# Kernel optimization log

Measured on AMD Instinct MI355X. Metric: run time of the kernel, lower is better.

The kernel has to match this reference:

```python
import jax, jax.numpy as jnp
import numpy as np

B, S, D, E = 4, 1024, 1024, 4
HID = 2816  # multiple_of * ceil(int(2*4*D/3) / multiple_of), multiple_of=256
COND = 1024  # min(D, 1024)
NORM_EPS = 1e-5  # block norms
LN_EPS = 1e-5    # q_norm/k_norm default eps


def setup_inputs() -> dict:
    key = jax.random.key(0)
    ks = jax.random.split(key, 16)
    w = lambda i, shape: jax.random.normal(ks[i], shape, jnp.float32) * 0.02
    return {
        'x': jax.random.normal(ks[0], (B, S, D), jnp.float32),
        'freqs_cis': jax.random.normal(ks[1], (S, 32), jnp.float32),  # unused by the block
        'adaln_input': jax.random.normal(ks[2], (B, COND), jnp.float32),
        'wq': w(3, (D, D)), 'wk': w(4, (D, D)), 'wv': w(5, (D, D)), 'wo': w(6, (D, D)),
        'q_norm_w': jnp.ones((D,), jnp.float32), 'q_norm_b': jnp.zeros((D,), jnp.float32),
        'k_norm_w': jnp.ones((D,), jnp.float32), 'k_norm_b': jnp.zeros((D,), jnp.float32),
        'attn_norm_w': jnp.ones((D,), jnp.float32), 'attn_norm_b': jnp.zeros((D,), jnp.float32),
        'ffn_norm_w': jnp.ones((D,), jnp.float32), 'ffn_norm_b': jnp.zeros((D,), jnp.float32),
        'w1': w(7, (E, D, HID)), 'w2': w(8, (E, HID, D)), 'w3': w(9, (E, D, HID)),
        'router_w': w(10, (D, E)), 'router_b': jnp.zeros((E,), jnp.float32),
        'ada_w': w(11, (COND, 6 * D)), 'ada_b': jnp.zeros((6 * D,), jnp.float32),
    }


def _ln(x, w, b, eps):
    mu = jnp.mean(x, -1, keepdims=True)
    var = jnp.mean((x - mu) ** 2, -1, keepdims=True)
    return (x - mu) * jax.lax.rsqrt(var + eps) * w + b


def _attention(x, wq, wk, wv, wo, qn_w, qn_b, kn_w, kn_b):
    # NOTE: this module attends over the FEATURE dim (no head split, no 1/sqrt(d) scale):
    # xq,xk,xv are permuted to [B, D, S]; scores are [B, D, D].
    q = _ln(x @ wq, qn_w, qn_b, LN_EPS)
    k = _ln(x @ wk, kn_w, kn_b, LN_EPS)
    v = x @ wv
    scores = jnp.einsum('bsd,bse->bde', q, k)          # [B, D, D]
    attn = jax.nn.softmax(scores, axis=-1)
    out = jnp.einsum('bde,bse->bsd', attn, v)          # [B, S, D]
    return out @ wo


def _moe(x, w1, w2, w3, router_w, router_b):
    logits = x @ router_w + router_b                   # [B, S, E]
    # F.normalize default dim=1 -> L2-normalize along the SEQUENCE dim (faithful quirk)
    nrm = jnp.sqrt(jnp.sum(logits * logits, axis=1, keepdims=True))
    logits = logits / jnp.maximum(nrm, 1e-12)
    probs = jax.nn.softmax(logits, axis=-1)
    topw, topi = jax.lax.top_k(probs, 2)
    # dense combine weights [B,S,E]: identical math to the masked gather/scatter dispatch
    combine = jnp.sum(jax.nn.one_hot(topi, E, dtype=x.dtype) * topw[..., None], axis=-2)
    h1 = jnp.einsum('bsd,edh->ebsh', x, w1)
    h3 = jnp.einsum('bsd,edh->ebsh', x, w3)
    out_e = jnp.einsum('ebsh,ehd->ebsd', jnp.sin(h1) * h3, w2)
    moe = jnp.einsum('bse,ebsd->bsd', combine, out_e)
    avg = jnp.mean(probs, axis=0)                      # [S, E] (mean over batch dim only)
    aux = jnp.sum((1.0 / E - avg) ** 2)
    return moe, aux


def reference(x, freqs_cis, adaln_input, wq, wk, wv, wo, q_norm_w, q_norm_b, k_norm_w,
              k_norm_b, attn_norm_w, attn_norm_b, ffn_norm_w, ffn_norm_b, w1, w2, w3,
              router_w, router_b, ada_w, ada_b):
    ada = jax.nn.silu(adaln_input) @ ada_w + ada_b     # [B, 6D]
    shift_msa, scale_msa, gate_msa, shift_mlp, scale_mlp, gate_mlp = jnp.split(ada, 6, axis=1)
    h = _ln(x, attn_norm_w, attn_norm_b, NORM_EPS)
    h = h * (1.0 + scale_msa[:, None, :]) + shift_msa[:, None, :]
    x = x + gate_msa[:, None, :] * _attention(h, wq, wk, wv, wo, q_norm_w, q_norm_b, k_norm_w, k_norm_b)
    h = _ln(x, ffn_norm_w, ffn_norm_b, NORM_EPS)
    h = h * (1.0 + scale_mlp[:, None, :]) + shift_mlp[:, None, :]
    # MoE path REPLACES x (no residual, gate_mlp unused) — faithful to the source
    x, aux = _moe(h, w1, w2, w3, router_w, router_b)
    return x, aux
```

## Files before the change

kernel.cpp:

```cpp
#include <hip/hip_runtime.h>
#include <hip/hip_bf16.h>
#include <math.h>

#define BB 4
#define SS 1024
#define DD 1024
#define EE 4
#define HID 2816
#define HC 1408
#define SIXD 6144
#define NSLOT 8704
#define NMB 68

typedef __bf16 v8bf __attribute__((ext_vector_type(8)));
typedef float  v4f  __attribute__((ext_vector_type(4)));

__device__ __forceinline__ ushort f2bf(float f) {
    union { float f; unsigned u; } v; v.f = f;
    unsigned r = v.u + 0x7fff + ((v.u >> 16) & 1);
    return (ushort)(r >> 16);
}
__device__ __forceinline__ float bf2f(ushort u) {
    union { unsigned u; float f; } v; v.u = ((unsigned)u) << 16;
    return v.f;
}
__device__ __forceinline__ void split_bf(float x, ushort& h, ushort& l) {
    h = f2bf(x);
    l = f2bf(x - bf2f(h));
}
__device__ __forceinline__ void gload16(const void* g, void* l) {
    __builtin_amdgcn_global_load_lds((const __attribute__((address_space(1))) void*)g,
                                     (__attribute__((address_space(3))) void*)l, 16, 0, 0);
}
template<int N> __device__ __forceinline__ void wait_vm() {
    __builtin_amdgcn_s_waitcnt((N & 15) | (0x7 << 4) | (0xF << 8) | ((N >> 4) << 14));
}

__device__ __forceinline__ void xcd_remap(int& bx, int& by) {
    const int gx = gridDim.x, gy = gridDim.y;
    const int nwg = gx * gy;
    const int wid = bx + gx * by;
    const int q = nwg >> 3, r = nwg & 7;
    const int xcd = wid & 7, loc = wid >> 3;
    const int pos = (xcd < r) ? (xcd * (q + 1) + loc)
                              : (r * (q + 1) + (xcd - r) * q + loc);
    bx = pos % gx; by = pos / gx;
}

__device__ __forceinline__ void xcd_remap_cm(int& bx, int& by) {
    const int gx = gridDim.x, gy = gridDim.y;
    const int nwg = gx * gy;
    const int wid = bx + gx * by;
    const int q = nwg >> 3, r = nwg & 7;
    const int xcd = wid & 7, loc = wid >> 3;
    const int pos = (xcd < r) ? (xcd * (q + 1) + loc)
                              : (r * (q + 1) + (xcd - r) * q + loc);
    bx = pos / gy; by = pos % gy;
}

__device__ __forceinline__ void moe_remap(int& bx, int& by) {
    const int gx = gridDim.x, gy = gridDim.y;
    const int total = gx * gy;
    const int wid = bx + gx * by;
    if ((total & 7) || (gx & 1)) { xcd_remap(bx, by); return; }
    const int q = total >> 3;
    const int pos = (wid & 7) * q + (wid >> 3);
    const int NG = gx >> 1;
    const int gh = NG * gy;
    const int nh = pos / gh, r = pos % gh;
    by = r / NG;
    bx = nh * NG + (r % NG);
}

template<int EPI, bool SPLIT>
__global__ __launch_bounds__(256, 2) void mgemm(
    const ushort* __restrict__ Ah, const ushort* __restrict__ Al,
    const ushort* __restrict__ Bh, const ushort* __restrict__ Bl,
    void* __restrict__ Cv, ushort* __restrict__ C2,
    const float* __restrict__ f1, const float* __restrict__ f2,
    int K, int lda, int ldb, int ldc,
    long sA, long sB, long sC)
{
    constexpr int STG = SPLIT ? 12288 : 6144;
    constexpr int BH  = SPLIT ? 8192 : 4096;
    constexpr int L   = SPLIT ? 6 : 3;
    __shared__ __align__(16) ushort smem[3 * STG];

    const int tid  = threadIdx.x;
    const int wv   = tid >> 6, lane = tid & 63;

    int bx = blockIdx.x, by = blockIdx.y;
    xcd_remap(bx, by);
    const int n0 = bx * 64;
    const int m0 = by * 128;
    const long zA = (long)blockIdx.z * sA;
    const long zB = (long)blockIdx.z * sB;
    const long zC = (long)blockIdx.z * sC;

    const int lrow = tid >> 2;
    const int skq  = ((tid & 3) ^ ((tid >> 3) & 3)) * 8;
    const int lm   = lane & 15;
    const int qs   = (((lane >> 4) ^ ((lm >> 1) & 3)) * 8);

    v4f acc[2][4];
    const v4f vzero = {0.f, 0.f, 0.f, 0.f};
    #pragma unroll
    for (int i = 0; i < 2; ++i)
        #pragma unroll
        for (int j = 0; j < 4; ++j) acc[i][j] = vzero;

    auto issue = [&](int kt, int st) {
        const long kk = (long)kt * 32 + skq;
        ushort* base = smem + st * STG;
        #pragma unroll
        for (int c = 0; c < 2; ++c) {
            const int row  = c * 64 + lrow;
            const int loff = (c * 64 + wv * 16) * 32;
            gload16(Ah + zA + (long)(m0 + row) * lda + kk, base + loff);
            if (SPLIT)
                gload16(Al + zA + (long)(m0 + row) * lda + kk, base + 4096 + loff);
        }
        {
            const int loff = wv * 16 * 32;
            gload16(Bh + zB + (long)(n0 + lrow) * ldb + kk, base + BH + loff);
            if (SPLIT)
                gload16(Bl + zB + (long)(n0 + lrow) * ldb + kk, base + BH + 2048 + loff);
        }
    };

    const int nk = K / 32;
    issue(0, 0);
    if (nk > 1) issue(1, 1);
    for (int kt = 0; kt < nk; ++kt) {
        if (kt + 1 < nk) wait_vm<L>(); else wait_vm<0>();
        __builtin_amdgcn_s_barrier();
        if (kt + 2 < nk) issue(kt + 2, (kt + 2) % 3);
        const ushort* As = smem + (kt % 3) * STG;
        v8bf a[2], b[4];
        #pragma unroll
        for (int i = 0; i < 2; ++i) a[i] = *(const v8bf*)(As + (wv*32 + 16*i + lm) * 32 + qs);
        #pragma unroll
        for (int j = 0; j < 4; ++j) b[j] = *(const v8bf*)(As + BH + (16*j + lm) * 32 + qs);
        #pragma unroll
        for (int i = 0; i < 2; ++i)
            #pragma unroll
            for (int j = 0; j < 4; ++j)
                acc[i][j] = __builtin_amdgcn_mfma_f32_16x16x32_bf16(a[i], b[j], acc[i][j], 0, 0, 0);
        if (SPLIT) {
            v8bf al[2], bl[4];
            #pragma unroll
            for (int i = 0; i < 2; ++i) al[i] = *(const v8bf*)(As + 4096 + (wv*32 + 16*i + lm) * 32 + qs);
            #pragma unroll
            for (int j = 0; j < 4; ++j) bl[j] = *(const v8bf*)(As + BH + 2048 + (16*j + lm) * 32 + qs);
            #pragma unroll
            for (int i = 0; i < 2; ++i)
                #pragma unroll
                for (int j = 0; j < 4; ++j) {
                    acc[i][j] = __builtin_amdgcn_mfma_f32_16x16x32_bf16(a[i],  bl[j], acc[i][j], 0, 0, 0);
                    acc[i][j] = __builtin_amdgcn_mfma_f32_16x16x32_bf16(al[i], b[j],  acc[i][j], 0, 0, 0);
                }
        }
    }

    const int r0 = (lane >> 4) * 4;
    #pragma unroll
    for (int i = 0; i < 2; ++i) {
        #pragma unroll
        for (int j = 0; j < 4; ++j) {
            const int colg = n0 + 16*j + lm;
            #pragma unroll
            for (int r = 0; r < 4; ++r) {
                const long rowg = (long)(m0 + wv*32 + 16*i + r0 + r);
                const long idx  = zC + rowg * ldc + colg;
                const float val = acc[i][j][r];
                if (EPI == 0) {
                    ((float*)Cv)[idx] = val;
                } else if (EPI == 2) {
                    ((float*)Cv)[idx] = f1[idx] + f2[(rowg >> 10) * SIXD + 2048 + colg] * val;
                } else if (EPI == 5) {
                    ushort h, l; split_bf(val, h, l);
                    ((ushort*)Cv)[idx] = h;
                    C2[idx] = l;
                }
            }
        }
    }
}

__global__ __launch_bounds__(256, 2) void mgemm_qkv(
    const ushort* __restrict__ Ah, const ushort* __restrict__ Al,
    const ushort* __restrict__ Bqh, const ushort* __restrict__ Bql,
    const ushort* __restrict__ Bkh, const ushort* __restrict__ Bkl,
    const ushort* __restrict__ Bvh, const ushort* __restrict__ Bvl,
    float* __restrict__ Cq, float* __restrict__ Ck,
    ushort* __restrict__ Cvh, ushort* __restrict__ Cvl)
{
    constexpr int STG = 20480;
    __shared__ __align__(16) ushort smem[2 * STG];

    const int tid  = threadIdx.x;
    const int wv   = tid >> 6, lane = tid & 63;

    int bx = blockIdx.x, by = blockIdx.y;
    xcd_remap(bx, by);
    const int n0 = bx * 64, m0 = by * 128;

    const int lrow = tid >> 2;
    const int skq  = ((tid & 3) ^ ((tid >> 3) & 3)) * 8;
    const int lm   = lane & 15;
    const int qs   = (((lane >> 4) ^ ((lm >> 1) & 3)) * 8);

    const ushort* Bh_[3] = {Bqh, Bkh, Bvh};
    const ushort* Bl_[3] = {Bql, Bkl, Bvl};

    v4f aq[2][4], ak[2][4], av[2][4];
    const v4f vzero = {0.f, 0.f, 0.f, 0.f};
    #pragma unroll
    for (int i = 0; i < 2; ++i)
        #pragma unroll
        for (int j = 0; j < 4; ++j) { aq[i][j] = vzero; ak[i][j] = vzero; av[i][j] = vzero; }

    auto issue = [&](int kt, int st) {
        const long kk = (long)kt * 32 + skq;
        ushort* base = smem + st * STG;
        #pragma unroll
        for (int c = 0; c < 2; ++c) {
            const int row  = c * 64 + lrow;
            const int loff = (c * 64 + wv * 16) * 32;
            gload16(Ah + (long)(m0 + row) * 1024 + kk, base + loff);
            gload16(Al + (long)(m0 + row) * 1024 + kk, base + 4096 + loff);
        }
        const int loff = wv * 16 * 32;
        #pragma unroll
        for (int m = 0; m < 3; ++m) {
            gload16(Bh_[m] + (long)(n0 + lrow) * 1024 + kk, base + 8192 + m * 4096 + loff);
            gload16(Bl_[m] + (long)(n0 + lrow) * 1024 + kk, base + 8192 + m * 4096 + 2048 + loff);
        }
    };

    issue(0, 0);
    #pragma unroll 1
    for (int kt = 0; kt < 32; ++kt) {
        const int stg = kt & 1;
        if (kt) __builtin_amdgcn_s_barrier();
        const bool hasNext = (kt + 1 < 32);
        if (hasNext) issue(kt + 1, stg ^ 1);
        if (hasNext) wait_vm<10>(); else wait_vm<0>();
        __builtin_amdgcn_s_barrier();
        const ushort* As = smem + stg * STG;
        v8bf a[2], alo[2];
        #pragma unroll
        for (int i = 0; i < 2; ++i) {
            a[i]   = *(const v8bf*)(As + (wv*32 + 16*i + lm) * 32 + qs);
            alo[i] = *(const v8bf*)(As + 4096 + (wv*32 + 16*i + lm) * 32 + qs);
        }
        auto mat = [&](const ushort* Bs, v4f (&acc)[2][4]) {
            v8bf b[4], bl[4];
            #pragma unroll
            for (int j = 0; j < 4; ++j) {
                b[j]  = *(const v8bf*)(Bs + (16*j + lm) * 32 + qs);
                bl[j] = *(const v8bf*)(Bs + 2048 + (16*j + lm) * 32 + qs);
            }
            #pragma unroll
            for (int i = 0; i < 2; ++i)
                #pragma unroll
                for (int j = 0; j < 4; ++j) {
                    acc[i][j] = __builtin_amdgcn_mfma_f32_16x16x32_bf16(a[i],   b[j],  acc[i][j], 0, 0, 0);
                    acc[i][j] = __builtin_amdgcn_mfma_f32_16x16x32_bf16(a[i],   bl[j], acc[i][j], 0, 0, 0);
                    acc[i][j] = __builtin_amdgcn_mfma_f32_16x16x32_bf16(alo[i], b[j],  acc[i][j], 0, 0, 0);
                }
        };
        mat(As + 8192,        aq);
        mat(As + 8192 + 4096, ak);
        mat(As + 8192 + 8192, av);
    }

    const int r0 = (lane >> 4) * 4;
    #pragma unroll
    for (int i = 0; i < 2; ++i)
        #pragma unroll
        for (int j = 0; j < 4; ++j) {
            const int colg = n0 + 16*j + lm;
            #pragma unroll
            for (int r = 0; r < 4; ++r) {
                const long rowg = (long)(m0 + wv*32 + 16*i + r0 + r);
                const long idx  = rowg * 1024 + colg;
                Cq[idx] = aq[i][j][r];
                Ck[idx] = ak[i][j][r];
                ushort h, l; split_bf(av[i][j][r], h, l);
                Cvh[idx] = h;
                Cvl[idx] = l;
            }
        }
}

__global__ __launch_bounds__(512, 2) void mgemm_h1h3(
    const ushort* __restrict__ Ah, const ushort* __restrict__ B1,
    const ushort* __restrict__ B2, ushort* __restrict__ Cb,
    const int* __restrict__ tokidx, const int* __restrict__ mbe,
    const int* __restrict__ mbm, long sB)
{
    constexpr int STG = 12288;
    __shared__ __align__(16) ushort smem[3 * STG];

    const int tid  = threadIdx.x;
    const int wv   = tid >> 6, lane = tid & 63;
    const int wr   = wv >> 2, wc = wv & 3;

    int bx = blockIdx.x, by = blockIdx.y;
    xcd_remap_cm(bx, by);
    const int n0 = bx * 128;
    const int eexp = mbe[by];
    if (eexp < 0) return;
    const int m0 = mbm[by];
    const long zB = (long)eexp * sB;

    const int lrow = tid >> 2;
    const int skq  = ((tid & 3) ^ ((tid >> 3) & 3)) * 8;
    const int lm   = lane & 15;
    const int qs   = (((lane >> 4) ^ ((lm >> 1) & 3)) * 8);

    const int t = tokidx[m0 + lrow];
    const long arow = (t < 0) ? 0 : (long)t;

    v4f acc[4][2], acc2[4][2];
    const v4f vzero = {0.f, 0.f, 0.f, 0.f};
    #pragma unroll
    for (int i = 0; i < 4; ++i)
        #pragma unroll
        for (int j = 0; j < 2; ++j) { acc[i][j] = vzero; acc2[i][j] = vzero; }

    auto issue = [&](int kt, int st) {
        const long kk = (long)kt * 32 + skq;
        ushort* base = smem + st * STG;
        const int loff = wv * 16 * 32;
        gload16(Ah + arow * 1024 + kk, base + loff);
        gload16(B1 + zB + (long)(n0 + lrow) * 1024 + kk, base + 4096 + loff);
        gload16(B2 + zB + (long)(n0 + lrow) * 1024 + kk, base + 8192 + loff);
    };

    issue(0, 0);
    issue(1, 1);
    int s_cur = 0, s_nxt = 2;
    #pragma unroll 1
    for (int kt = 0; kt < 32; ++kt) {
        if (kt + 1 < 32) wait_vm<3>(); else wait_vm<0>();
        __builtin_amdgcn_s_barrier();
        if (kt + 2 < 32) issue(kt + 2, s_nxt);
        const ushort* As = smem + s_cur * STG;
        v8bf a[4], b1[2], b2[2];
        #pragma unroll
        for (int i = 0; i < 4; ++i) a[i] = *(const v8bf*)(As + (wr*64 + 16*i + lm) * 32 + qs);
        #pragma unroll
        for (int j = 0; j < 2; ++j) {
            b1[j] = *(const v8bf*)(As + 4096 + (wc*32 + 16*j + lm) * 32 + qs);
            b2[j] = *(const v8bf*)(As + 8192 + (wc*32 + 16*j + lm) * 32 + qs);
        }
        #pragma unroll
        for (int i = 0; i < 4; ++i)
            #pragma unroll
            for (int j = 0; j < 2; ++j) {
                acc[i][j]  = __builtin_amdgcn_mfma_f32_16x16x32_bf16(a[i], b1[j], acc[i][j],  0, 0, 0);
                acc2[i][j] = __builtin_amdgcn_mfma_f32_16x16x32_bf16(a[i], b2[j], acc2[i][j], 0, 0, 0);
            }
        s_cur = (s_cur == 2) ? 0 : s_cur + 1;
        s_nxt = (s_nxt == 2) ? 0 : s_nxt + 1;
    }

    const int r0 = (lane >> 4) * 4;
    #pragma unroll
    for (int i = 0; i < 4; ++i)
        #pragma unroll
        for (int j = 0; j < 2; ++j) {
            const int colg = n0 + wc*32 + 16*j + lm;
            #pragma unroll
            for (int r = 0; r < 4; ++r) {
                const long rowg = (long)(m0 + wr*64 + 16*i + r0 + r);
                Cb[rowg * HC + colg] = f2bf(sinf(acc[i][j][r]) * acc2[i][j][r]);
            }
        }
}

__global__ __launch_bounds__(256, 2) void mgemm_w2(
    const ushort* __restrict__ Ah, const ushort* __restrict__ Bh,
    float* __restrict__ Cv, const float* __restrict__ comb,
    const int* __restrict__ tokidx, const int* __restrict__ mbe,
    const int* __restrict__ mbm, long sB)
{
    constexpr int STG = 8192;
    __shared__ __align__(16) ushort smem[3 * STG];

    const int tid  = threadIdx.x;
    const int wv   = tid >> 6, lane = tid & 63;
    const int wr   = wv >> 1, wc = wv & 1;

    int bx = blockIdx.x, by = blockIdx.y;
    moe_remap(bx, by);
    const int n0 = bx * 128;
    const int eexp = mbe[by];
    if (eexp < 0) return;
    const int m0 = mbm[by];
    const long zB = (long)eexp * sB;

    const int lrow = tid >> 2;
    const int skq  = ((tid & 3) ^ ((tid >> 3) & 3)) * 8;
    const int lm   = lane & 15;
    const int qs   = (((lane >> 4) ^ ((lm >> 1) & 3)) * 8);

    v4f acc[4][4];
    const v4f vzero = {0.f, 0.f, 0.f, 0.f};
    #pragma unroll
    for (int i = 0; i < 4; ++i)
        #pragma unroll
        for (int j = 0; j < 4; ++j) acc[i][j] = vzero;

    auto issue = [&](int kt, int st) {
        const long kk = (long)kt * 32 + skq;
        ushort* base = smem + st * STG;
        #pragma unroll
        for (int c = 0; c < 2; ++c) {
            const int loff = (c * 64 + wv * 16) * 32;
            gload16(Ah + (long)(m0 + c * 64 + lrow) * HC + kk, base + loff);
            gload16(Bh + zB + (long)(n0 + c * 64 + lrow) * HC + kk, base + 4096 + loff);
        }
    };

    const int nk = HC / 32;
    issue(0, 0);
    issue(1, 1);
    int s_cur = 0, s_nxt = 2;
    #pragma unroll 1
    for (int kt = 0; kt < nk; ++kt) {
        if (kt + 1 < nk) wait_vm<4>(); else wait_vm<0>();
        __builtin_amdgcn_s_barrier();
        if (kt + 2 < nk) issue(kt + 2, s_nxt);
        const ushort* As = smem + s_cur * STG;
        v8bf a[4], b[4];
        #pragma unroll
        for (int i = 0; i < 4; ++i) a[i] = *(const v8bf*)(As + (wr*64 + 16*i + lm) * 32 + qs);
        #pragma unroll
        for (int j = 0; j < 4; ++j) b[j] = *(const v8bf*)(As + 4096 + (wc*64 + 16*j + lm) * 32 + qs);
        #pragma unroll
        for (int i = 0; i < 4; ++i)
            #pragma unroll
            for (int j = 0; j < 4; ++j)
                acc[i][j] = __builtin_amdgcn_mfma_f32_16x16x32_bf16(a[i], b[j], acc[i][j], 0, 0, 0);
        s_cur = (s_cur == 2) ? 0 : s_cur + 1;
        s_nxt = (s_nxt == 2) ? 0 : s_nxt + 1;
    }

    const int r0 = (lane >> 4) * 4;
    #pragma unroll
    for (int i = 0; i < 4; ++i)
        #pragma unroll
        for (int r = 0; r < 4; ++r) {
            const int rowg = m0 + wr*64 + 16*i + r0 + r;
            const int t = tokidx[rowg];
            if (t >= 0) {
                const float cw = comb[t * 4 + eexp];
                #pragma unroll
                for (int j = 0; j < 4; ++j)
                    atomicAdd(Cv + (long)t * 1024 + n0 + wc*64 + 16*j + lm, cw * acc[i][j][r]);
            }
        }
}

template<bool SP>
__global__ __launch_bounds__(256) void transp(
    const float* __restrict__ in, ushort* __restrict__ oh, ushort* __restrict__ ol,
    int ldin, int ldout, long sIn, long sOut)
{
    __shared__ float T[64][65];
    const int n0 = blockIdx.x * 64, k0 = blockIdx.y * 64;
    in += (long)blockIdx.z * sIn;
    oh += (long)blockIdx.z * sOut;
    if (SP) ol += (long)blockIdx.z * sOut;
    const int t = threadIdx.x;
    const int rr = t >> 4, c4 = (t & 15) * 4;
    #pragma unroll
    for (int p = 0; p < 4; ++p) {
        const int r = rr + p * 16;
        const float4 v = *(const float4*)(in + (long)(k0 + r) * ldin + n0 + c4);
        T[c4+0][r] = v.x; T[c4+1][r] = v.y; T[c4+2][r] = v.z; T[c4+3][r] = v.w;
    }
    __syncthreads();
    #pragma unroll
    for (int p = 0; p < 4; ++p) {
        const int idx = t + 256 * p;
        const int n = idx >> 4, c = (idx & 15) * 4;
        ushort4 wh, wl;
        float x0 = T[n][c], x1 = T[n][c+1], x2 = T[n][c+2], x3 = T[n][c+3];
        if (SP) {
            split_bf(x0, wh.x, wl.x); split_bf(x1, wh.y, wl.y);
            split_bf(x2, wh.z, wl.z); split_bf(x3, wh.w, wl.w);
        } else {
            wh.x = f2bf(x0); wh.y = f2bf(x1); wh.z = f2bf(x2); wh.w = f2bf(x3);
        }
        *(ushort4*)(oh + (long)(n0 + n) * ldout + k0 + c) = wh;
        if (SP) *(ushort4*)(ol + (long)(n0 + n) * ldout + k0 + c) = wl;
    }
}

__global__ __launch_bounds__(256) void ada_kernel(
    const float* __restrict__ adaln, const float* __restrict__ aw,
    const float* __restrict__ ab, float* __restrict__ ada)
{
    __shared__ float s[DD];
    const int b = blockIdx.y;
    const int tid = threadIdx.x;
    for (int i = tid; i < DD; i += 256) {
        const float v = adaln[(long)b * DD + i];
        s[i] = v / (1.f + expf(-v));
    }
    __syncthreads();
    const int n = blockIdx.x * 256 + tid;
    float acc = 0.f;
    for (int k = 0; k < DD; ++k) acc += s[k] * aw[(long)k * SIXD + n];
    ada[(long)b * SIXD + n] = acc + ab[n];
}

template<int OUT, bool MOD>
__global__ __launch_bounds__(256) void ln_kernel(
    const float* __restrict__ x, const float* __restrict__ w, const float* __restrict__ bias,
    const float* __restrict__ ada, int scale_off, int shift_off,
    float* __restrict__ o32, ushort* __restrict__ oh, ushort* __restrict__ ol, float eps)
{
    const int row = blockIdx.x;
    const int b = row >> 10;
    const int tid = threadIdx.x;
    const float* xr = x + (long)row * DD;
    float v[4]; float s = 0.f, q = 0.f;
    #pragma unroll
    for (int i = 0; i < 4; ++i) { v[i] = xr[tid + 256*i]; s += v[i]; q += v[i]*v[i]; }
    __shared__ float rs_[256], rq_[256];
    rs_[tid] = s; rq_[tid] = q; __syncthreads();
    for (int off = 128; off > 0; off >>= 1) {
        if (tid < off) { rs_[tid] += rs_[tid+off]; rq_[tid] += rq_[tid+off]; }
        __syncthreads();
    }
    const float mu  = rs_[0] * (1.f/DD);
    const float var = rq_[0] * (1.f/DD) - mu*mu;
    const float rstd = rsqrtf(var + eps);
    const float* ar = ada + (long)b * SIXD;
    #pragma unroll
    for (int i = 0; i < 4; ++i) {
        const int d = tid + 256*i;
        float y = (v[i] - mu) * rstd * w[d] + bias[d];
        if (MOD) y = y * (1.f + ar[scale_off + d]) + ar[shift_off + d];
        const long idx = (long)row * DD + d;
        if (OUT == 0) o32[idx] = y;
        else if (OUT == 1) { ushort h, l; split_bf(y, h, l); oh[idx] = h; ol[idx] = l; }
        else oh[idx] = f2bf(y);
    }
}

__global__ __launch_bounds__(256) void softmax_split(
    const float* __restrict__ in, ushort* __restrict__ oh, ushort* __restrict__ ol)
{
    const long row = blockIdx.x;
    const float* p = in + row * 1024;
    const int tid = threadIdx.x;
    float v[4]; float mx = -INFINITY;
    #pragma unroll
    for (int i = 0; i < 4; ++i) { v[i] = p[tid + 256*i]; mx = fmaxf(mx, v[i]); }
    __shared__ float red[256];
    red[tid] = mx; __syncthreads();
    for (int off = 128; off > 0; off >>= 1) {
        if (tid < off) red[tid] = fmaxf(red[tid], red[tid+off]);
        __syncthreads();
    }
    const float rowmax = red[0];
    __syncthreads();
    float s = 0.f;
    #pragma unroll
    for (int i = 0; i < 4; ++i) { v[i] = expf(v[i] - rowmax); s += v[i]; }
    red[tid] = s; __syncthreads();
    for (int off = 128; off > 0; off >>= 1) {
        if (tid < off) red[tid] += red[tid+off];
        __syncthreads();
    }
    const float inv = 1.f / red[0];
    #pragma unroll
    for (int i = 0; i < 4; ++i) {
        ushort h, l; split_bf(v[i] * inv, h, l);
        oh[row*1024 + tid + 256*i] = h;
        ol[row*1024 + tid + 256*i] = l;
    }
}

__global__ __launch_bounds__(256) void ln_router(
    const float* __restrict__ x2, const float* __restrict__ fw, const float* __restrict__ fb,
    const float* __restrict__ ada, const float* __restrict__ rw, const float* __restrict__ rb,
    float* __restrict__ logits, ushort* __restrict__ oh)
{
    const int row = blockIdx.x;
    const int b = row >> 10;
    const int tid = threadIdx.x;
    const float* xr = x2 + (long)row * DD;
    float v[4]; float s = 0.f, q = 0.f;
    #pragma unroll
    for (int i = 0; i < 4; ++i) { v[i] = xr[tid + 256*i]; s += v[i]; q += v[i]*v[i]; }
    __shared__ float rs_[256], rq_[256];
    rs_[tid] = s; rq_[tid] = q; __syncthreads();
    for (int off = 128; off > 0; off >>= 1) {
        if (tid < off) { rs_[tid] += rs_[tid+off]; rq_[tid] += rq_[tid+off]; }
        __syncthreads();
    }
    const float mu  = rs_[0] * (1.f/DD);
    const float var = rq_[0] * (1.f/DD) - mu*mu;
    const float rstd = rsqrtf(var + 1e-5f);
    const float* ar = ada + (long)b * SIXD;
    float acc[4] = {0.f, 0.f, 0.f, 0.f};
    #pragma unroll
    for (int i = 0; i < 4; ++i) {
        const int d = tid + 256*i;
        float h = (v[i] - mu) * rstd * fw[d] + fb[d];
        h = h * (1.f + ar[4096 + d]) + ar[3072 + d];
        oh[(long)row * DD + d] = f2bf(h);
        const float* r4 = rw + (long)d * 4;
        acc[0] += h*r4[0]; acc[1] += h*r4[1]; acc[2] += h*r4[2]; acc[3] += h*r4[3];
    }
    __syncthreads();
    __shared__ float red[256];
    for (int e = 0; e < EE; ++e) {
        red[tid] = acc[e]; __syncthreads();
        for (int off = 128; off > 0; off >>= 1) {
            if (tid < off) red[tid] += red[tid+off];
            __syncthreads();
        }
        if (tid == 0) logits[(long)row * EE + e] = red[0] + rb[e];
        __syncthreads();
    }
}

__global__ __launch_bounds__(1024) void router_all(
    const float* __restrict__ logits, float* __restrict__ comb,
    float* __restrict__ auxout, int* __restrict__ tokidx,
    int* __restrict__ mbe, int* __restrict__ mbm)
{
    __shared__ float pl[16384];
    __shared__ float red[1024];
    __shared__ float nrm_l[16];
    __shared__ int lc[4], loff[4], lpos[4];
    const int tid = threadIdx.x;
    const int wv = tid >> 6, ln = tid & 63;
    {
        const int b = wv >> 2, e = wv & 3;
        float s = 0.f;
        for (int it = 0; it < 16; ++it) {
            const float v = logits[(((long)b << 10) + ln + (it << 6)) * 4 + e];
            s += v * v;
        }
        for (int off = 32; off > 0; off >>= 1) s += __shfl_down(s, off, 64);
        if (ln == 0) nrm_l[wv] = fmaxf(sqrtf(s), 1e-12f);
    }
    if (tid < 4) lc[tid] = 0;
    __syncthreads();
    float cloc[4][4];
    const int rbase = tid * 4;
    for (int rr = 0; rr < 4; ++rr) {
        const int row = rbase + rr;
        const int b = row >> 10;
        float l[4], p[4];
        #pragma unroll
        for (int e = 0; e < 4; ++e) l[e] = logits[(long)row*4 + e] / nrm_l[b*4 + e];
        const float mx = fmaxf(fmaxf(l[0], l[1]), fmaxf(l[2], l[3]));
        float s = 0.f;
        #pragma unroll
        for (int e = 0; e < 4; ++e) { p[e] = expf(l[e] - mx); s += p[e]; }
        const float inv = 1.f / s;
        #pragma unroll
        for (int e = 0; e < 4; ++e) { p[e] *= inv; pl[row*4 + e] = p[e]; }
        int i1 = 0;
        #pragma unroll
        for (int e = 1; e < 4; ++e) if (p[e] > p[i1]) i1 = e;
        int i2 = (i1 == 0) ? 1 : 0;
        #pragma unroll
        for (int e = 0; e < 4; ++e) if (e != i1 && p[e] > p[i2]) i2 = e;
        #pragma unroll
        for (int e = 0; e < 4; ++e) {
            const float c = (e == i1) ? p[i1] : ((e == i2) ? p[i2] : 0.f);
            cloc[rr][e] = c;
            comb[(long)row*4 + e] = c;
            if (c > 0.f) atomicAdd(&lc[e], 1);
        }
    }
    __syncthreads();
    float acc = 0.f;
    for (int i = tid; i < 4096; i += 1024) {
        const int s = i >> 2, e = i & 3;
        const float avg = 0.25f * (pl[s*4+e] + pl[(1024+s)*4+e] +
                                   pl[(2048+s)*4+e] + pl[(3072+s)*4+e]);
        const float d = 0.25f - avg;
        acc += d * d;
    }
    red[tid] = acc; __syncthreads();
    for (int off = 512; off > 0; off >>= 1) {
        if (tid < off) red[tid] += red[tid+off];
        __syncthreads();
    }
    if (tid == 0) auxout[0] = red[0];
    if (tid == 0) {
        int off0 = 0, nb = 0;
        for (int e = 0; e < 4; ++e) {
            loff[e] = off0; lpos[e] = 0;
            const int mb = (lc[e] + 127) >> 7;
            for (int k = 0; k < mb; ++k) { mbe[nb] = e; mbm[nb] = off0 + k*128; ++nb; }
            off0 += mb << 7;
        }
        for (; nb < NMB; ++nb) { mbe[nb] = -1; mbm[nb] = 0; }
    }
    for (int i = tid; i < NSLOT; i += 1024) tokidx[i] = -1;
    __syncthreads();
    for (int rr = 0; rr < 4; ++rr) {
        const int row = rbase + rr;
        #pragma unroll
        for (int e = 0; e < 4; ++e)
            if (cloc[rr][e] > 0.f) {
                const int s = atomicAdd(&lpos[e], 1);
                tokidx[loff[e] + s] = row;
            }
    }
}

__global__ __launch_bounds__(256) void zero_kernel(float4* __restrict__ out)
{
    out[(long)blockIdx.x * 256 + threadIdx.x] = float4{0.f, 0.f, 0.f, 0.f};
}

extern "C" void kernel_launch(void* const* d_in, const int* in_sizes, int n_in,
                              void* d_out, int out_size, void* d_ws, size_t ws_size,
                              hipStream_t stream)
{
    (void)in_sizes; (void)n_in; (void)out_size; (void)ws_size;
    const float* x     = (const float*)d_in[0];
    const float* adaln = (const float*)d_in[2];
    const float* wq    = (const float*)d_in[3];
    const float* wk    = (const float*)d_in[4];
    const float* wv    = (const float*)d_in[5];
    const float* wo    = (const float*)d_in[6];
    const float* qn_w  = (const float*)d_in[7];
    const float* qn_b  = (const float*)d_in[8];
    const float* kn_w  = (const float*)d_in[9];
    const float* kn_b  = (const float*)d_in[10];
    const float* an_w  = (const float*)d_in[11];
    const float* an_b  = (const float*)d_in[12];
    const float* fn_w  = (const float*)d_in[13];
    const float* fn_b  = (const float*)d_in[14];
    const float* w1    = (const float*)d_in[15];
    const float* w2    = (const float*)d_in[16];
    const float* w3    = (const float*)d_in[17];
    const float* rw    = (const float*)d_in[18];
    const float* rb    = (const float*)d_in[19];
    const float* aw    = (const float*)d_in[20];
    const float* ab    = (const float*)d_in[21];
    float* out = (float*)d_out;

    const long NBAT = (long)SS * DD;
    const long NBUF = (long)BB * SS * DD;
#define MB(x) ((long)(x) * 1048576L)

    char* P = (char*)d_ws;
    float* ada    = (float*)P;
    float* logits = (float*)(P + 98304);
    float* comb   = logits + 16384;
    int*   tokidx = (int*)(comb + 16384);
    int*   mbe    = tokidx + NSLOT;
    int*   mbm    = mbe + NMB;

    char* A0 = P + MB(1);
    ushort* wqT_h = (ushort*)(A0 + MB(0));  ushort* wqT_l = (ushort*)(A0 + MB(2));
    ushort* wkT_h = (ushort*)(A0 + MB(4));  ushort* wkT_l = (ushort*)(A0 + MB(6));
    ushort* wvT_h = (ushort*)(A0 + MB(8));  ushort* wvT_l = (ushort*)(A0 + MB(10));
    ushort* woT_h = (ushort*)(A0 + MB(0));  ushort* woT_l = (ushort*)(A0 + MB(2));
    ushort* w1Tc  = (ushort*)(A0 + MB(0));
    ushort* h_h   = (ushort*)(A0 + MB(12)); ushort* h_l  = (ushort*)(A0 + MB(20));
    ushort* qT_h  = (ushort*)(A0 + MB(12)); ushort* qT_l = (ushort*)(A0 + MB(20));
    ushort* ao_h  = (ushort*)(A0 + MB(12)); ushort* ao_l = (ushort*)(A0 + MB(20));
    ushort* actb  = (ushort*)(A0 + MB(12));
    float*  q32   = (float*) (A0 + MB(28));
    float*  sc    = (float*) (A0 + MB(28));
    float*  x2    = (float*) (A0 + MB(28));
    ushort* v_h   = (ushort*)(A0 + MB(44)); ushort* v_l  = (ushort*)(A0 + MB(52));
    float*  k32   = (float*) (A0 + MB(60));
    ushort* at_h  = (ushort*)(A0 + MB(60)); ushort* at_l = (ushort*)(A0 + MB(68));
    ushort* w3Tc  = (ushort*)(A0 + MB(60));
    ushort* kT_h  = (ushort*)(A0 + MB(76)); ushort* kT_l = (ushort*)(A0 + MB(84));
    ushort* h2bf  = (ushort*)(A0 + MB(76));
    ushort* w2Tc  = (ushort*)(A0 + MB(84));

    const dim3 blk(256);

    ada_kernel<<<dim3(SIXD/256, BB), blk, 0, stream>>>(adaln, aw, ab, ada);

    transp<true><<<dim3(16,16,1), blk, 0, stream>>>(wq, wqT_h, wqT_l, 1024, 1024, 0, 0);
    transp<true><<<dim3(16,16,1), blk, 0, stream>>>(wk, wkT_h, wkT_l, 1024, 1024, 0, 0);
    transp<true><<<dim3(16,16,1), blk, 0, stream>>>(wv, wvT_h, wvT_l, 1024, 1024, 0, 0);

    ln_kernel<1,true><<<4096, blk, 0, stream>>>(x, an_w, an_b, ada, 1024, 0,
                                                nullptr, h_h, h_l, 1e-5f);

    mgemm_qkv<<<dim3(16,32), blk, 0, stream>>>(
        h_h, h_l, wqT_h, wqT_l, wkT_h, wkT_l, wvT_h, wvT_l,
        q32, k32, v_h, v_l);

    ln_kernel<0,false><<<4096, blk, 0, stream>>>(q32, qn_w, qn_b, ada, 0, 0, q32, nullptr, nullptr, 1e-5f);
    transp<true><<<dim3(16,16,BB), blk, 0, stream>>>(q32, qT_h, qT_l, 1024, 1024, NBAT, NBAT);

    ln_kernel<0,false><<<4096, blk, 0, stream>>>(k32, kn_w, kn_b, ada, 0, 0, k32, nullptr, nullptr, 1e-5f);
    transp<true><<<dim3(16,16,BB), blk, 0, stream>>>(k32, kT_h, kT_l, 1024, 1024, NBAT, NBAT);

    transp<true><<<dim3(16,16,1), blk, 0, stream>>>(wo, woT_h, woT_l, 1024, 1024, 0, 0);

    mgemm<0,true><<<dim3(16,8,BB), blk, 0, stream>>>(
        qT_h, qT_l, kT_h, kT_l, sc, nullptr, nullptr, nullptr,
        1024, 1024, 1024, 1024, NBAT, NBAT, NBAT);

    softmax_split<<<4096, blk, 0, stream>>>(sc, at_h, at_l);

    mgemm<5,true><<<dim3(16,8,BB), blk, 0, stream>>>(
        v_h, v_l, at_h, at_l, ao_h, ao_l, nullptr, nullptr,
        1024, 1024, 1024, 1024, NBAT, NBAT, NBAT);

    mgemm<2,true><<<dim3(16,32,1), blk, 0, stream>>>(
        ao_h, ao_l, woT_h, woT_l, x2, nullptr, x, ada,
        1024, 1024, 1024, 1024, 0, 0, 0);

    ln_router<<<4096, blk, 0, stream>>>(x2, fn_w, fn_b, ada, rw, rb, logits, h2bf);

    router_all<<<1, dim3(1024), 0, stream>>>(logits, comb, out + NBUF, tokidx, mbe, mbm);
    zero_kernel<<<dim3(4096), blk, 0, stream>>>((float4*)out);

    for (int c = 0; c < HID/HC; ++c) {
        transp<false><<<dim3(22,16,4), blk, 0, stream>>>(
            w1 + (long)c*HC, w1Tc, nullptr, HID, 1024, (long)DD*HID, (long)HC*1024);
        transp<false><<<dim3(22,16,4), blk, 0, stream>>>(
            w3 + (long)c*HC, w3Tc, nullptr, HID, 1024, (long)DD*HID, (long)HC*1024);
        transp<false><<<dim3(16,22,4), blk, 0, stream>>>(
            w2 + (long)c*HC*DD, w2Tc, nullptr, DD, HC, (long)HID*DD, (long)DD*HC);
        mgemm_h1h3<<<dim3(11, NMB), dim3(512), 0, stream>>>(
            h2bf, w1Tc, w3Tc, actb, tokidx, mbe, mbm, (long)HC*1024);
        mgemm_w2<<<dim3(8, NMB), blk, 0, stream>>>(
            actb, w2Tc, out, comb, tokidx, mbe, mbm, (long)DD*HC);
    }
#undef MB
}
```

Measured before the change: 814.7 us.

## Enlarge split-bf16 GEMM tile to 128x128 with double-buffered pipeline

Reworks the generic split-precision GEMM, used for scores, attn·V and the output projection, from a 128x64 tile with a 3-stage ring to a 128x128 tile. Waves are arranged 2x2, each owning a 64x64 sub-tile, and shared memory holds two stages. The larger tile raises MFMA work per LDS/global byte and halves the block count. In exchange it needs more accumulator registers (64 floats per lane), may cut occupancy, has shallower prefetch, and leaves fewer blocks (256) to fill the CUs.

```diff
diff --git a/kernel.cpp b/kernel.cpp
--- a/kernel.cpp
+++ b/kernel.cpp
@@ -72,7 +72,7 @@
     bx = nh * NG + (r % NG);
 }
 
-template<int EPI, bool SPLIT>
+template<int EPI>
 __global__ __launch_bounds__(256, 2) void mgemm(
     const ushort* __restrict__ Ah, const ushort* __restrict__ Al,
     const ushort* __restrict__ Bh, const ushort* __restrict__ Bl,
@@ -81,17 +81,16 @@
     int K, int lda, int ldb, int ldc,
     long sA, long sB, long sC)
 {
-    constexpr int STG = SPLIT ? 12288 : 6144;
-    constexpr int BH  = SPLIT ? 8192 : 4096;
-    constexpr int L   = SPLIT ? 6 : 3;
-    __shared__ __align__(16) ushort smem[3 * STG];
+    constexpr int STG = 16384;
+    __shared__ __align__(16) ushort smem[2 * STG];
 
     const int tid  = threadIdx.x;
     const int wv   = tid >> 6, lane = tid & 63;
+    const int wr   = wv >> 1, wc = wv & 1;
 
     int bx = blockIdx.x, by = blockIdx.y;
     xcd_remap(bx, by);
-    const int n0 = bx * 64;
+    const int n0 = bx * 128;
     const int m0 = by * 128;
     const long zA = (long)blockIdx.z * sA;
     const long zB = (long)blockIdx.z * sB;
@@ -102,10 +101,10 @@
     const int lm   = lane & 15;
     const int qs   = (((lane >> 4) ^ ((lm >> 1) & 3)) * 8);
 
-    v4f acc[2][4];
+    v4f acc[4][4];
     const v4f vzero = {0.f, 0.f, 0.f, 0.f};
     #pragma unroll
-    for (int i = 0; i < 2; ++i)
+    for (int i = 0; i < 4; ++i)
         #pragma unroll
         for (int j = 0; j < 4; ++j) acc[i][j] = vzero;
 
@@ -114,63 +113,55 @@
         ushort* base = smem + st * STG;
         #pragma unroll
         for (int c = 0; c < 2; ++c) {
-            const int row  = c * 64 + lrow;
             const int loff = (c * 64 + wv * 16) * 32;
-            gload16(Ah + zA + (long)(m0 + row) * lda + kk, base + loff);
-            if (SPLIT)
-                gload16(Al + zA + (long)(m0 + row) * lda + kk, base + 4096 + loff);
-        }
-        {
-            const int loff = wv * 16 * 32;
-            gload16(Bh + zB + (long)(n0 + lrow) * ldb + kk, base + BH + loff);
-            if (SPLIT)
-                gload16(Bl + zB + (long)(n0 + lrow) * ldb + kk, base + BH + 2048 + loff);
+            gload16(Ah + zA + (long)(m0 + c * 64 + lrow) * lda + kk, base + loff);
+            gload16(Al + zA + (long)(m0 + c * 64 + lrow) * lda + kk, base + 4096 + loff);
+            gload16(Bh + zB + (long)(n0 + c * 64 + lrow) * ldb + kk, base + 8192 + loff);
+            gload16(Bl + zB + (long)(n0 + c * 64 + lrow) * ldb + kk, base + 12288 + loff);
         }
     };
 
     const int nk = K / 32;
     issue(0, 0);
-    if (nk > 1) issue(1, 1);
+    #pragma unroll 1
     for (int kt = 0; kt < nk; ++kt) {
-        if (kt + 1 < nk) wait_vm<L>(); else wait_vm<0>();
+        const int stg = kt & 1;
+        if (kt) __builtin_amdgcn_s_barrier();
+        const bool hasNext = (kt + 1 < nk);
+        if (hasNext) issue(kt + 1, stg ^ 1);
+        if (hasNext) wait_vm<8>(); else wait_vm<0>();
         __builtin_amdgcn_s_barrier();
-        if (kt + 2 < nk) issue(kt + 2, (kt + 2) % 3);
-        const ushort* As = smem + (kt % 3) * STG;
-        v8bf a[2], b[4];
-        #pragma unroll
-        for (int i = 0; i < 2; ++i) a[i] = *(const v8bf*)(As + (wv*32 + 16*i + lm) * 32 + qs);
-        #pragma unroll
-        for (int j = 0; j < 4; ++j) b[j] = *(const v8bf*)(As + BH + (16*j + lm) * 32 + qs);
-        #pragma unroll
-        for (int i = 0; i < 2; ++i)
+        const ushort* As = smem + stg * STG;
+        v8bf a[4], alo[4], b[4], bl[4];
+        #pragma unroll
+        for (int i = 0; i < 4; ++i) {
+            a[i]   = *(const v8bf*)(As + (wr*64 + 16*i + lm) * 32 + qs);
+            alo[i] = *(const v8bf*)(As + 4096 + (wr*64 + 16*i + lm) * 32 + qs);
+        }
+        #pragma unroll
+        for (int j = 0; j < 4; ++j) {
+            b[j]  = *(const v8bf*)(As + 8192 + (wc*64 + 16*j + lm) * 32 + qs);
+            bl[j] = *(const v8bf*)(As + 12288 + (wc*64 + 16*j + lm) * 32 + qs);
+        }
+        #pragma unroll
+        for (int i = 0; i < 4; ++i)
             #pragma unroll
-            for (int j = 0; j < 4; ++j)
-                acc[i][j] = __builtin_amdgcn_mfma_f32_16x16x32_bf16(a[i], b[j], acc[i][j], 0, 0, 0);
-        if (SPLIT) {
-            v8bf al[2], bl[4];
-            #pragma unroll
-            for (int i = 0; i < 2; ++i) al[i] = *(const v8bf*)(As + 4096 + (wv*32 + 16*i + lm) * 32 + qs);
-            #pragma unroll
-            for (int j = 0; j < 4; ++j) bl[j] = *(const v8bf*)(As + BH + 2048 + (16*j + lm) * 32 + qs);
-            #pragma unroll
-            for (int i = 0; i < 2; ++i)
-                #pragma unroll
-                for (int j = 0; j < 4; ++j) {
-                    acc[i][j] = __builtin_amdgcn_mfma_f32_16x16x32_bf16(a[i],  bl[j], acc[i][j], 0, 0, 0);
-                    acc[i][j] = __builtin_amdgcn_mfma_f32_16x16x32_bf16(al[i], b[j],  acc[i][j], 0, 0, 0);
-                }
-        }
+            for (int j = 0; j < 4; ++j) {
+                acc[i][j] = __builtin_amdgcn_mfma_f32_16x16x32_bf16(a[i],   b[j],  acc[i][j], 0, 0, 0);
+                acc[i][j] = __builtin_amdgcn_mfma_f32_16x16x32_bf16(a[i],   bl[j], acc[i][j], 0, 0, 0);
+                acc[i][j] = __builtin_amdgcn_mfma_f32_16x16x32_bf16(alo[i], b[j],  acc[i][j], 0, 0, 0);
+            }
     }
 
     const int r0 = (lane >> 4) * 4;
     #pragma unroll
-    for (int i = 0; i < 2; ++i) {
+    for (int i = 0; i < 4; ++i) {
         #pragma unroll
         for (int j = 0; j < 4; ++j) {
-            const int colg = n0 + 16*j + lm;
+            const int colg = n0 + wc*64 + 16*j + lm;
             #pragma unroll
             for (int r = 0; r < 4; ++r) {
-                const long rowg = (long)(m0 + wv*32 + 16*i + r0 + r);
+                const long rowg = (long)(m0 + wr*64 + 16*i + r0 + r);
                 const long idx  = zC + rowg * ldc + colg;
                 const float val = acc[i][j][r];
                 if (EPI == 0) {
@@ -812,17 +803,17 @@
 
     transp<true><<<dim3(16,16,1), blk, 0, stream>>>(wo, woT_h, woT_l, 1024, 1024, 0, 0);
 
-    mgemm<0,true><<<dim3(16,8,BB), blk, 0, stream>>>(
+    mgemm<0><<<dim3(8,8,BB), blk, 0, stream>>>(
         qT_h, qT_l, kT_h, kT_l, sc, nullptr, nullptr, nullptr,
         1024, 1024, 1024, 1024, NBAT, NBAT, NBAT);
 
     softmax_split<<<4096, blk, 0, stream>>>(sc, at_h, at_l);
 
-    mgemm<5,true><<<dim3(16,8,BB), blk, 0, stream>>>(
+    mgemm<5><<<dim3(8,8,BB), blk, 0, stream>>>(
         v_h, v_l, at_h, at_l, ao_h, ao_l, nullptr, nullptr,
         1024, 1024, 1024, 1024, NBAT, NBAT, NBAT);
 
-    mgemm<2,true><<<dim3(16,32,1), blk, 0, stream>>>(
+    mgemm<2><<<dim3(8,32,1), blk, 0, stream>>>(
         ao_h, ao_l, woT_h, woT_l, x2, nullptr, x, ada,
         1024, 1024, 1024, 1024, 0, 0, 0);
 
```

Result: no change. 803.8 us (-1.3%).
